# Kernel tuning notes

Hardware: AMD Instinct MI355X
Metric: run time of the kernel (lower is better)

Reference implementation:

```python
import jax, jax.numpy as jnp
import numpy as np

N = 100000   # nodes
E = 1000000  # edges (avg degree 10)
F_IN, H1, H2, C = 128, 64, 64, 16


def setup_inputs() -> dict:
    key = jax.random.key(0)
    ks = jax.random.split(key, 10)
    x = jax.random.normal(ks[0], (N, F_IN), dtype=jnp.float32)
    edge_src = jax.random.randint(ks[1], (E,), 0, N, dtype=jnp.int32)
    edge_dst = jax.random.randint(ks[2], (E,), 0, N, dtype=jnp.int32)
    # normalized-adjacency-like positive edge weights (~1/deg scale)
    edge_val = jax.random.uniform(ks[3], (E,), dtype=jnp.float32) * 0.1
    def glorot(k, fan_in, fan_out):
        s = np.float32(1.0 / np.sqrt(fan_in))
        return jax.random.normal(k, (fan_in, fan_out), dtype=jnp.float32) * s
    W1 = glorot(ks[4], F_IN, H1)
    W2 = glorot(ks[5], H1, H2)
    W3 = glorot(ks[6], H2, C)
    b1 = jnp.zeros((H1,), jnp.float32)
    b2 = jnp.zeros((H2,), jnp.float32)
    b3 = jnp.zeros((C,), jnp.float32)
    return {"x": x, "edge_val": edge_val, "W1": W1, "b1": b1,
            "W2": W2, "b2": b2, "W3": W3, "b3": b3,
            "edge_src": edge_src, "edge_dst": edge_dst}


def gcn_layer(h, W, b, edge_src, edge_dst, edge_val):
    # support = h @ W ; out = spmm(adj, support) + b
    support = h @ W                                  # [N, d_out]
    msg = support[edge_src] * edge_val[:, None]      # [E, d_out] gather + scale
    agg = jax.ops.segment_sum(msg, edge_dst, num_segments=N)  # scatter-add
    return agg + b


def reference(x, edge_val, W1, b1, W2, b2, W3, b3, edge_src, edge_dst):
    # eval mode: F.dropout(training=False) is identity
    h = jax.nn.relu(gcn_layer(x, W1, b1, edge_src, edge_dst, edge_val))
    h = jax.nn.relu(gcn_layer(h, W2, b2, edge_src, edge_dst, edge_val))
    return gcn_layer(h, W3, b3, edge_src, edge_dst, edge_val)  # [N, C] logits
```

## Files before the change

### kernel.cpp

```cpp
#include <hip/hip_runtime.h>
#include <stdint.h>

#define N_NODES 100000
#define N_EDGES 1000000
#define NBUCK 98
#define CAP 12288

typedef __attribute__((ext_vector_type(8))) __bf16 bf16x8;
typedef __attribute__((ext_vector_type(4))) float f32x4;

static __device__ __forceinline__ float bf2f(unsigned short u) {
    return __uint_as_float(((unsigned int)u) << 16);
}
static __device__ __forceinline__ unsigned short f2bf(float f) {
    unsigned int u = __float_as_uint(f);
    unsigned int r = (u + 0x7FFFu + ((u >> 16) & 1u)) >> 16;
    return (unsigned short)r;
}
static __device__ __forceinline__ float4 ld4_half(const unsigned short* p) {
    ushort4 u = *(const ushort4*)p;
    return make_float4(bf2f(u.x), bf2f(u.y), bf2f(u.z), bf2f(u.w));
}
static __device__ __forceinline__ void st4_half(unsigned short* p, float4 f) {
    ushort4 u;
    u.x = f2bf(f.x); u.y = f2bf(f.y); u.z = f2bf(f.z); u.w = f2bf(f.w);
    *(ushort4*)p = u;
}
static __device__ __forceinline__ void st8_half(unsigned short* p, const float* f) {
    int4 u;
    u.x = (int)(((unsigned)f2bf(f[0])) | (((unsigned)f2bf(f[1])) << 16));
    u.y = (int)(((unsigned)f2bf(f[2])) | (((unsigned)f2bf(f[3])) << 16));
    u.z = (int)(((unsigned)f2bf(f[4])) | (((unsigned)f2bf(f[5])) << 16));
    u.w = (int)(((unsigned)f2bf(f[6])) | (((unsigned)f2bf(f[7])) << 16));
    *(int4*)p = u;
}

static __device__ __forceinline__ float ldf(const void* p, size_t i, int bf) {
    return bf ? bf2f(((const unsigned short*)p)[i]) : ((const float*)p)[i];
}
static __device__ __forceinline__ float4 ldf4(const void* p, size_t i, int bf) {
    if (bf) return ld4_half((const unsigned short*)p + i);
    return *(const float4*)((const float*)p + i);
}

__global__ __launch_bounds__(256) void detect_kernel(const unsigned short* __restrict__ xs,
                                                     int* __restrict__ flag,
                                                     int* __restrict__ bcursor) {
    __shared__ int sz;
    if (threadIdx.x == 0) sz = 0;
    __syncthreads();
    int z = 0;
    for (int i = threadIdx.x; i < 1024; i += 256) {
        float av = fabsf(bf2f(xs[2 * i]));
        if (!(av <= 1048576.0f) || (av != 0.0f && av < 9.5367431640625e-07f)) z++;
    }
    atomicAdd(&sz, z);
    if (threadIdx.x < NBUCK) bcursor[threadIdx.x] = threadIdx.x * CAP;
    __syncthreads();
    if (threadIdx.x == 0) *flag = (sz > 256) ? 0 : 1;
}

__global__ __launch_bounds__(256) void part_kernel(const int* __restrict__ src,
                                                   const int* __restrict__ dst,
                                                   const void* __restrict__ val,
                                                   int* __restrict__ bcursor,
                                                   int2* __restrict__ part,
                                                   const int* __restrict__ flagp) {
    __shared__ int cnt[NBUCK];
    __shared__ int base[NBUCK];
    const int bf = *flagp;
    const int tid = threadIdx.x;
    const int e0 = blockIdx.x * 2048;
    for (int i = tid; i < NBUCK; i += 256) cnt[i] = 0;
    __syncthreads();
    int rank[8], bkt[8], pk[8], vb[8];
#pragma unroll
    for (int i = 0; i < 8; ++i) {
        int e = e0 + i * 256 + tid;
        bkt[i] = -1;
        if (e < N_EDGES) {
            int d = dst[e];
            int b = d >> 10;
            bkt[i] = b;
            pk[i] = src[e] | ((d & 1023) << 17);
            vb[i] = __float_as_int(ldf(val, e, bf));
            rank[i] = atomicAdd(&cnt[b], 1);
        }
    }
    __syncthreads();
    for (int i = tid; i < NBUCK; i += 256) {
        int c = cnt[i];
        base[i] = c ? atomicAdd(&bcursor[i], c) : 0;
    }
    __syncthreads();
#pragma unroll
    for (int i = 0; i < 8; ++i) {
        if (bkt[i] >= 0) part[(size_t)base[bkt[i]] + rank[i]] = make_int2(pk[i], vb[i]);
    }
}

__global__ __launch_bounds__(512) void place_kernel(const int* __restrict__ bcursor,
                                                    const int2* __restrict__ part,
                                                    int* __restrict__ row_start,
                                                    int2* __restrict__ csr_rec) {
    __shared__ int cnt[1024];
    __shared__ int sums[512];
    __shared__ int sh_s, sh_cnt, sh_total;
    const int tid = threadIdx.x;
    const int b = blockIdx.x;
    const int row0 = b << 10;
    const int nrows = min(1024, N_NODES - row0);

    if (tid < 128) sums[tid] = (tid < NBUCK) ? (bcursor[tid] - tid * CAP) : 0;
    __syncthreads();
    for (int off = 1; off < 128; off <<= 1) {
        int t = 0;
        if (tid < 128 && tid >= off) t = sums[tid - off];
        __syncthreads();
        if (tid < 128 && tid >= off) sums[tid] += t;
        __syncthreads();
    }
    if (tid == 0) {
        sh_s = (b > 0) ? sums[b - 1] : 0;
        sh_cnt = bcursor[b] - b * CAP;
        sh_total = sums[NBUCK - 1];
    }
    __syncthreads();
    const int s = sh_s;
    const int cb = sh_cnt;
    const int ps = b * CAP;
    const int total = sh_total;

    for (int i = tid; i < 1024; i += 512) cnt[i] = 0;
    __syncthreads();
    for (int j = tid; j < cb; j += 512) {
        unsigned p = (unsigned)part[ps + j].x;
        atomicAdd(&cnt[p >> 17], 1);
    }
    __syncthreads();
    int a0 = cnt[2 * tid], a1 = cnt[2 * tid + 1];
    int ts = a0 + a1;
    sums[tid] = ts;
    __syncthreads();
    for (int off = 1; off < 512; off <<= 1) {
        int t = 0;
        if (tid >= off) t = sums[tid - off];
        __syncthreads();
        if (tid >= off) sums[tid] += t;
        __syncthreads();
    }
    int excl = sums[tid] - ts;
    cnt[2 * tid] = s + excl;
    cnt[2 * tid + 1] = s + excl + a0;
    if (2 * tid < nrows)     row_start[row0 + 2 * tid] = s + excl;
    if (2 * tid + 1 < nrows) row_start[row0 + 2 * tid + 1] = s + excl + a0;
    if (b == NBUCK - 1 && tid == 0) row_start[N_NODES] = total;
    __syncthreads();
    for (int j = tid; j < cb; j += 512) {
        int2 r = part[ps + j];
        unsigned p = (unsigned)r.x;
        int pos = atomicAdd(&cnt[p >> 17], 1);
        csr_rec[pos] = make_int2((int)(p & 0x1FFFFu), r.y);
    }
}

static __device__ __forceinline__ void duo_gather64(const unsigned short* __restrict__ supc,
                                                    const int2* __restrict__ csr_rec,
                                                    int s, int b1, int e,
                                                    float a0[8], float a1[8]) {
    if (s >= e) return;
    int2 r[8];
#pragma unroll
    for (int t = 0; t < 8; ++t) r[t] = csr_rec[min(s + t, e - 1)];
    for (int j = s; j < e; j += 8) {
        int4 sp[8];
#pragma unroll
        for (int t = 0; t < 8; ++t) sp[t] = *(const int4*)(supc + (size_t)r[t].x * 64);
        float wv[8];
#pragma unroll
        for (int t = 0; t < 8; ++t) wv[t] = (j + t < e) ? __int_as_float(r[t].y) : 0.0f;
        int jn = j + 8;
        if (jn < e) {
#pragma unroll
            for (int t = 0; t < 8; ++t) r[t] = csr_rec[min(jn + t, e - 1)];
        }
#pragma unroll
        for (int t = 0; t < 8; ++t) {
            float w0 = (j + t < b1) ? wv[t] : 0.0f;
            float w1 = wv[t] - w0;
            int q[4] = {sp[t].x, sp[t].y, sp[t].z, sp[t].w};
#pragma unroll
            for (int c = 0; c < 4; ++c) {
                float flo = __uint_as_float(((unsigned)q[c]) << 16);
                float fhi = __uint_as_float(((unsigned)q[c]) & 0xffff0000u);
                a0[2 * c]     += w0 * flo; a0[2 * c + 1] += w0 * fhi;
                a1[2 * c]     += w1 * flo; a1[2 * c + 1] += w1 * fhi;
            }
        }
    }
}

static __device__ __forceinline__ void quad_gather16(const unsigned short* __restrict__ supc,
                                                     const int2* __restrict__ csr_rec,
                                                     int s, int b1, int b2, int b3, int e,
                                                     float a[4][8]) {
    if (s >= e) return;
    int2 r[8];
#pragma unroll
    for (int t = 0; t < 8; ++t) r[t] = csr_rec[min(s + t, e - 1)];
    for (int j = s; j < e; j += 8) {
        int4 sp[8];
#pragma unroll
        for (int t = 0; t < 8; ++t) sp[t] = *(const int4*)(supc + (size_t)r[t].x * 16);
        float wv[8];
#pragma unroll
        for (int t = 0; t < 8; ++t) wv[t] = (j + t < e) ? __int_as_float(r[t].y) : 0.0f;
        int jn = j + 8;
        if (jn < e) {
#pragma unroll
            for (int t = 0; t < 8; ++t) r[t] = csr_rec[min(jn + t, e - 1)];
        }
#pragma unroll
        for (int t = 0; t < 8; ++t) {
            int idx = j + t;
            float c0 = (idx < b1) ? wv[t] : 0.0f;
            float c1 = (idx < b2) ? wv[t] : 0.0f;
            float c2 = (idx < b3) ? wv[t] : 0.0f;
            float w0 = c0, w1 = c1 - c0, w2 = c2 - c1, w3 = wv[t] - c2;
            int q[4] = {sp[t].x, sp[t].y, sp[t].z, sp[t].w};
#pragma unroll
            for (int c = 0; c < 4; ++c) {
                float flo = __uint_as_float(((unsigned)q[c]) << 16);
                float fhi = __uint_as_float(((unsigned)q[c]) & 0xffff0000u);
                a[0][2 * c] += w0 * flo; a[0][2 * c + 1] += w0 * fhi;
                a[1][2 * c] += w1 * flo; a[1][2 * c + 1] += w1 * fhi;
                a[2][2 * c] += w2 * flo; a[2][2 * c + 1] += w2 * fhi;
                a[3][2 * c] += w3 * flo; a[3][2 * c + 1] += w3 * fhi;
            }
        }
    }
}

template <int K, int M, bool DYNIN>
__global__ __launch_bounds__(256) void mgemm_kernel(const void* __restrict__ hv_,
                                                    const void* __restrict__ W,
                                                    unsigned short* __restrict__ out,
                                                    const int* __restrict__ flagp) {
    constexpr int KP = K + 8;
    constexpr int NC = M / 16;
    constexpr int NK = K / 32;

    __shared__ unsigned short wt[M][KP];

    const int bf = *flagp;
    const int tid = threadIdx.x;

    for (int i = tid; i < K * M; i += 256) {
        int k = i / M, m = i % M;
        wt[m][k] = f2bf(ldf(W, i, bf));
    }
    __syncthreads();

    const int lane = tid & 63;
    const int qd = lane >> 4;
    const int ln = lane & 15;
    const int wrow = (tid >> 6) * 16;
    const int tile = blockIdx.x;

    const int row = tile * 64 + wrow + ln;
    const bool ok = row < N_NODES;

    f32x4 acc[NC];
#pragma unroll
    for (int c = 0; c < NC; ++c) acc[c] = (f32x4){0.f, 0.f, 0.f, 0.f};

#pragma unroll
    for (int ks = 0; ks < NK; ++ks) {
        bf16x8 a;
        if (ok) {
            const size_t base = (size_t)row * K + ks * 32 + qd * 8;
            if (DYNIN && !bf) {
                const float* xp = (const float*)hv_ + base;
                float4 f0 = *(const float4*)xp;
                float4 f1 = *(const float4*)(xp + 4);
                ushort4 uu[2];
                uu[0].x = f2bf(f0.x); uu[0].y = f2bf(f0.y); uu[0].z = f2bf(f0.z); uu[0].w = f2bf(f0.w);
                uu[1].x = f2bf(f1.x); uu[1].y = f2bf(f1.y); uu[1].z = f2bf(f1.z); uu[1].w = f2bf(f1.w);
                a = *(const bf16x8*)uu;
            } else {
                a = *(const bf16x8*)((const unsigned short*)hv_ + base);
            }
        } else {
            a = (bf16x8)(__bf16)0.0f;
        }
#pragma unroll
        for (int c = 0; c < NC; ++c) {
            bf16x8 b = *(const bf16x8*)&wt[c * 16 + ln][ks * 32 + qd * 8];
            acc[c] = __builtin_amdgcn_mfma_f32_16x16x32_bf16(a, b, acc[c], 0, 0, 0);
        }
    }

#pragma unroll
    for (int c = 0; c < NC; ++c) {
#pragma unroll
        for (int r = 0; r < 4; ++r) {
            int orow = tile * 64 + wrow + qd * 4 + r;
            if (orow < N_NODES) out[(size_t)orow * M + c * 16 + ln] = f2bf(acc[c][r]);
        }
    }
}

template <int MOUT>
__global__ __launch_bounds__(256) void fused_kernel(const unsigned short* __restrict__ support,
                                                    const int* __restrict__ row_start,
                                                    const int2* __restrict__ csr_rec,
                                                    const void* __restrict__ bias,
                                                    const void* __restrict__ W,
                                                    unsigned short* __restrict__ out,
                                                    const int* __restrict__ flagp) {
    constexpr int K = 64, KP = 72;
    constexpr int NC = MOUT / 16;
    constexpr int NK = 2;

    __shared__ unsigned short agg[64][KP];
    __shared__ unsigned short wt[MOUT][KP];

    const int bf = *flagp;
    const int tid = threadIdx.x;

    for (int i = tid; i < K * MOUT; i += 256) {
        int k = i / MOUT, m = i % MOUT;
        wt[m][k] = f2bf(ldf(W, i, bf));
    }
    __syncthreads();

    const int lane = tid & 63;
    const int qd = lane >> 4;
    const int ln = lane & 15;
    const int wrow = (tid >> 6) * 16;

    const int grp = tid >> 3;
    const int cc = tid & 7;
    float bias8[8];
#pragma unroll
    for (int c = 0; c < 8; ++c) bias8[c] = ldf(bias, cc * 8 + c, bf);
    const unsigned short* supc = support + cc * 8;

    const int tile = blockIdx.x;
    const int r0 = tile * 64 + grp * 2;
    int s  = row_start[min(r0 + 0, N_NODES)];
    int b1 = row_start[min(r0 + 1, N_NODES)];
    int e  = row_start[min(r0 + 2, N_NODES)];

    float a0[8], a1[8];
#pragma unroll
    for (int c = 0; c < 8; ++c) { a0[c] = bias8[c]; a1[c] = bias8[c]; }
    duo_gather64(supc, csr_rec, s, b1, e, a0, a1);
#pragma unroll
    for (int c = 0; c < 8; ++c) {
        a0[c] = fmaxf(a0[c], 0.f);
        a1[c] = fmaxf(a1[c], 0.f);
    }
    st8_half(&agg[grp * 2 + 0][cc * 8], a0);
    st8_half(&agg[grp * 2 + 1][cc * 8], a1);
    __syncthreads();

    f32x4 macc[NC];
#pragma unroll
    for (int c = 0; c < NC; ++c) macc[c] = (f32x4){0.f, 0.f, 0.f, 0.f};
#pragma unroll
    for (int ks = 0; ks < NK; ++ks) {
        bf16x8 a = *(const bf16x8*)&agg[wrow + ln][ks * 32 + qd * 8];
#pragma unroll
        for (int c = 0; c < NC; ++c) {
            bf16x8 b = *(const bf16x8*)&wt[c * 16 + ln][ks * 32 + qd * 8];
            macc[c] = __builtin_amdgcn_mfma_f32_16x16x32_bf16(a, b, macc[c], 0, 0, 0);
        }
    }

#pragma unroll
    for (int c = 0; c < NC; ++c) {
#pragma unroll
        for (int r = 0; r < 4; ++r) {
            int orow = tile * 64 + wrow + qd * 4 + r;
            if (orow < N_NODES) out[(size_t)orow * MOUT + c * 16 + ln] = f2bf(macc[c][r]);
        }
    }
}

template <bool DYNOUT>
__global__ __launch_bounds__(256) void spmm16_kernel(const unsigned short* __restrict__ support,
                                                     const int* __restrict__ row_start,
                                                     const int2* __restrict__ csr_rec,
                                                     const void* __restrict__ bias,
                                                     void* __restrict__ out_,
                                                     const int* __restrict__ flagp) {
    constexpr int M = 16;
    int bf = *flagp;
    int tid = threadIdx.x;
    int grp = tid >> 1;
    int cc = tid & 1;
    int r0 = blockIdx.x * 512 + grp * 4;
    if (r0 >= N_NODES) return;
    int s  = row_start[min(r0 + 0, N_NODES)];
    int b1 = row_start[min(r0 + 1, N_NODES)];
    int b2 = row_start[min(r0 + 2, N_NODES)];
    int b3 = row_start[min(r0 + 3, N_NODES)];
    int e  = row_start[min(r0 + 4, N_NODES)];
    float a[4][8];
#pragma unroll
    for (int k = 0; k < 4; ++k)
#pragma unroll
        for (int c = 0; c < 8; ++c) a[k][c] = ldf(bias, cc * 8 + c, bf);
    quad_gather16(support + cc * 8, csr_rec, s, b1, b2, b3, e, a);
#pragma unroll
    for (int k = 0; k < 4; ++k) {
        int row = r0 + k;
        if (row < N_NODES) {
            if (DYNOUT && !bf) {
                float* op = (float*)out_ + (size_t)row * M + cc * 8;
                *(float4*)op = make_float4(a[k][0], a[k][1], a[k][2], a[k][3]);
                *(float4*)(op + 4) = make_float4(a[k][4], a[k][5], a[k][6], a[k][7]);
            } else {
                st8_half((unsigned short*)out_ + (size_t)row * M + cc * 8, a[k]);
            }
        }
    }
}

extern "C" void kernel_launch(void* const* d_in, const int* in_sizes, int n_in,
                              void* d_out, int out_size, void* d_ws, size_t ws_size,
                              hipStream_t stream) {
    (void)in_sizes; (void)n_in; (void)out_size; (void)ws_size;
    const void* x  = d_in[0];
    const void* ev = d_in[1];
    const void* W1 = d_in[2];
    const void* b1 = d_in[3];
    const void* W2 = d_in[4];
    const void* b2 = d_in[5];
    const void* W3 = d_in[6];
    const void* b3 = d_in[7];
    const int* esrc = (const int*)d_in[8];
    const int* edst = (const int*)d_in[9];

    char* ws = (char*)d_ws;
    size_t off = 0;
    auto alloc = [&](size_t bytes) -> void* {
        void* p = ws + off;
        off = (off + bytes + 255) & ~(size_t)255;
        return p;
    };
    unsigned short* A = (unsigned short*)alloc((size_t)N_NODES * 64 * 2);
    unsigned short* B = (unsigned short*)alloc((size_t)N_NODES * 64 * 2);
    int* row_start  = (int*)alloc((size_t)(N_NODES + 1) * 4);
    int* bcursor    = (int*)alloc(512);
    int2* csr_rec   = (int2*)alloc((size_t)N_EDGES * 8);
    int* flagp      = (int*)alloc(256);
    int2* part      = (int2*)A;

    detect_kernel<<<1, 256, 0, stream>>>((const unsigned short*)x, flagp, bcursor);

    part_kernel<<<(N_EDGES + 2047) / 2048, 256, 0, stream>>>(esrc, edst, ev, bcursor, part, flagp);
    place_kernel<<<NBUCK, 512, 0, stream>>>(bcursor, part, row_start, csr_rec);

    const int NT = (N_NODES + 63) / 64;

    mgemm_kernel<128, 64, true><<<NT, 256, 0, stream>>>(x, W1, A, flagp);
    fused_kernel<64><<<NT, 256, 0, stream>>>(A, row_start, csr_rec, b1, W2, B, flagp);
    fused_kernel<16><<<NT, 256, 0, stream>>>(B, row_start, csr_rec, b2, W3, A, flagp);
    spmm16_kernel<true><<<(N_NODES + 511) / 512, 256, 0, stream>>>(A, row_start, csr_rec, b3, d_out, flagp);
}
```

Measured before the change: 244.8 us.

## Fold dtype detection into partition, stage bucket writes in LDS, persist mgemm

Drops the separate single-block detect kernel: every partition block now recomputes the bf16/fp32 detection itself, and bucket cursors are zeroed with a memset. The partition kernel first sorts its records by bucket in shared memory, so the global scatter writes become contiguous runs instead of random 8-byte stores. The first GEMM switches to a fixed grid of 512 blocks that loop over tiles, which amortises the W staging across tiles. Float-to-bf16 packing now uses a hardware paired-conversion builtin when it is available. In exchange, each partition block pays for the redundant detection and the extra LDS scan and staging.

```diff
diff --git a/kernel.cpp b/kernel.cpp
--- a/kernel.cpp
+++ b/kernel.cpp
@@ -7,6 +7,7 @@
 #define CAP 12288
 
 typedef __attribute__((ext_vector_type(8))) __bf16 bf16x8;
+typedef __attribute__((ext_vector_type(2))) __bf16 bf16x2;
 typedef __attribute__((ext_vector_type(4))) float f32x4;
 
 static __device__ __forceinline__ float bf2f(unsigned short u) {
@@ -17,63 +18,77 @@
     unsigned int r = (u + 0x7FFFu + ((u >> 16) & 1u)) >> 16;
     return (unsigned short)r;
 }
+#if defined(__has_builtin)
+#if __has_builtin(__builtin_amdgcn_cvt_pk_bf16_f32)
+#define HAS_PK_BF16 1
+#endif
+#endif
+static __device__ __forceinline__ unsigned f2bf_pk(float a, float b) {
+#ifdef HAS_PK_BF16
+    bf16x2 v = __builtin_amdgcn_cvt_pk_bf16_f32(a, b);
+    unsigned u;
+    __builtin_memcpy(&u, &v, 4);
+    return u;
+#else
+    return ((unsigned)f2bf(a)) | (((unsigned)f2bf(b)) << 16);
+#endif
+}
 static __device__ __forceinline__ float4 ld4_half(const unsigned short* p) {
     ushort4 u = *(const ushort4*)p;
     return make_float4(bf2f(u.x), bf2f(u.y), bf2f(u.z), bf2f(u.w));
 }
 static __device__ __forceinline__ void st4_half(unsigned short* p, float4 f) {
-    ushort4 u;
-    u.x = f2bf(f.x); u.y = f2bf(f.y); u.z = f2bf(f.z); u.w = f2bf(f.w);
-    *(ushort4*)p = u;
+    uint2 u;
+    u.x = f2bf_pk(f.x, f.y);
+    u.y = f2bf_pk(f.z, f.w);
+    *(uint2*)p = u;
 }
 static __device__ __forceinline__ void st8_half(unsigned short* p, const float* f) {
-    int4 u;
-    u.x = (int)(((unsigned)f2bf(f[0])) | (((unsigned)f2bf(f[1])) << 16));
-    u.y = (int)(((unsigned)f2bf(f[2])) | (((unsigned)f2bf(f[3])) << 16));
-    u.z = (int)(((unsigned)f2bf(f[4])) | (((unsigned)f2bf(f[5])) << 16));
-    u.w = (int)(((unsigned)f2bf(f[6])) | (((unsigned)f2bf(f[7])) << 16));
-    *(int4*)p = u;
+    uint4 u;
+    u.x = f2bf_pk(f[0], f[1]);
+    u.y = f2bf_pk(f[2], f[3]);
+    u.z = f2bf_pk(f[4], f[5]);
+    u.w = f2bf_pk(f[6], f[7]);
+    *(uint4*)p = u;
 }
 
 static __device__ __forceinline__ float ldf(const void* p, size_t i, int bf) {
     return bf ? bf2f(((const unsigned short*)p)[i]) : ((const float*)p)[i];
-}
-static __device__ __forceinline__ float4 ldf4(const void* p, size_t i, int bf) {
-    if (bf) return ld4_half((const unsigned short*)p + i);
-    return *(const float4*)((const float*)p + i);
-}
-
-__global__ __launch_bounds__(256) void detect_kernel(const unsigned short* __restrict__ xs,
-                                                     int* __restrict__ flag,
-                                                     int* __restrict__ bcursor) {
-    __shared__ int sz;
-    if (threadIdx.x == 0) sz = 0;
-    __syncthreads();
-    int z = 0;
-    for (int i = threadIdx.x; i < 1024; i += 256) {
-        float av = fabsf(bf2f(xs[2 * i]));
-        if (!(av <= 1048576.0f) || (av != 0.0f && av < 9.5367431640625e-07f)) z++;
-    }
-    atomicAdd(&sz, z);
-    if (threadIdx.x < NBUCK) bcursor[threadIdx.x] = threadIdx.x * CAP;
-    __syncthreads();
-    if (threadIdx.x == 0) *flag = (sz > 256) ? 0 : 1;
 }
 
 __global__ __launch_bounds__(256) void part_kernel(const int* __restrict__ src,
                                                    const int* __restrict__ dst,
                                                    const void* __restrict__ val,
+                                                   const unsigned short* __restrict__ xs,
                                                    int* __restrict__ bcursor,
                                                    int2* __restrict__ part,
-                                                   const int* __restrict__ flagp) {
+                                                   int* __restrict__ flagp) {
     __shared__ int cnt[NBUCK];
-    __shared__ int base[NBUCK];
-    const int bf = *flagp;
+    __shared__ int lbase[NBUCK];
+    __shared__ int gbase[NBUCK];
+    __shared__ int sums[128];
+    __shared__ unsigned char bb[2048];
+    __shared__ int2 buf[2048];
+    __shared__ int sz;
+
     const int tid = threadIdx.x;
     const int e0 = blockIdx.x * 2048;
+
+    if (tid == 0) sz = 0;
     for (int i = tid; i < NBUCK; i += 256) cnt[i] = 0;
     __syncthreads();
-    int rank[8], bkt[8], pk[8], vb[8];
+    int z = 0;
+    for (int i = tid; i < 1024; i += 256) {
+        float av = fabsf(bf2f(xs[2 * i]));
+        if (!(av <= 1048576.0f) || (av != 0.0f && av < 9.5367431640625e-07f)) z++;
+    }
+    if (z) atomicAdd(&sz, z);
+    __syncthreads();
+    const int bf = (sz > 256) ? 0 : 1;
+    if (blockIdx.x == 0 && tid == 0) *flagp = bf;
+
+    int rank[8], bkt[8];
+    int2 rec[8];
 #pragma unroll
     for (int i = 0; i < 8; ++i) {
         int e = e0 + i * 256 + tid;
@@ -82,20 +97,40 @@
             int d = dst[e];
             int b = d >> 10;
             bkt[i] = b;
-            pk[i] = src[e] | ((d & 1023) << 17);
-            vb[i] = __float_as_int(ldf(val, e, bf));
+            rec[i] = make_int2(src[e] | ((d & 1023) << 17),
+                               __float_as_int(ldf(val, e, bf)));
             rank[i] = atomicAdd(&cnt[b], 1);
         }
     }
     __syncthreads();
-    for (int i = tid; i < NBUCK; i += 256) {
-        int c = cnt[i];
-        base[i] = c ? atomicAdd(&bcursor[i], c) : 0;
-    }
-    __syncthreads();
+    if (tid < 128) sums[tid] = (tid < NBUCK) ? cnt[tid] : 0;
+    __syncthreads();
+    for (int off = 1; off < 128; off <<= 1) {
+        int t = 0;
+        if (tid < 128 && tid >= off) t = sums[tid - off];
+        __syncthreads();
+        if (tid < 128 && tid >= off) sums[tid] += t;
+        __syncthreads();
+    }
+    if (tid < NBUCK) {
+        lbase[tid] = sums[tid] - cnt[tid];
+        gbase[tid] = cnt[tid] ? atomicAdd(&bcursor[tid], cnt[tid]) : 0;
+    }
+    __syncthreads();
+    const int total = sums[127];
 #pragma unroll
     for (int i = 0; i < 8; ++i) {
-        if (bkt[i] >= 0) part[(size_t)base[bkt[i]] + rank[i]] = make_int2(pk[i], vb[i]);
+        if (bkt[i] >= 0) {
+            int p = lbase[bkt[i]] + rank[i];
+            buf[p] = rec[i];
+            bb[p] = (unsigned char)bkt[i];
+        }
+    }
+    __syncthreads();
+    for (int j = tid; j < total; j += 256) {
+        int b = bb[j];
+        int k = j - lbase[b];
+        part[(size_t)b * CAP + gbase[b] + k] = buf[j];
     }
 }
 
@@ -111,7 +146,7 @@
     const int row0 = b << 10;
     const int nrows = min(1024, N_NODES - row0);
 
-    if (tid < 128) sums[tid] = (tid < NBUCK) ? (bcursor[tid] - tid * CAP) : 0;
+    if (tid < 128) sums[tid] = (tid < NBUCK) ? bcursor[tid] : 0;
     __syncthreads();
     for (int off = 1; off < 128; off <<= 1) {
         int t = 0;
@@ -122,7 +157,7 @@
     }
     if (tid == 0) {
         sh_s = (b > 0) ? sums[b - 1] : 0;
-        sh_cnt = bcursor[b] - b * CAP;
+        sh_cnt = bcursor[b];
         sh_total = sums[NBUCK - 1];
     }
     __syncthreads();
@@ -249,15 +284,19 @@
     constexpr int KP = K + 8;
     constexpr int NC = M / 16;
     constexpr int NK = K / 32;
+    constexpr int NT = (N_NODES + 63) / 64;
 
     __shared__ unsigned short wt[M][KP];
 
     const int bf = *flagp;
     const int tid = threadIdx.x;
 
-    for (int i = tid; i < K * M; i += 256) {
-        int k = i / M, m = i % M;
-        wt[m][k] = f2bf(ldf(W, i, bf));
+    for (int i = tid; i < M * (K / 2); i += 256) {
+        int m = i / (K / 2);
+        int kk = i % (K / 2);
+        float va = ldf(W, (size_t)(2 * kk) * M + m, bf);
+        float vb = ldf(W, (size_t)(2 * kk + 1) * M + m, bf);
+        *(unsigned*)&wt[m][2 * kk] = f2bf_pk(va, vb);
     }
     __syncthreads();
 
@@ -265,47 +304,50 @@
     const int qd = lane >> 4;
     const int ln = lane & 15;
     const int wrow = (tid >> 6) * 16;
-    const int tile = blockIdx.x;
-
-    const int row = tile * 64 + wrow + ln;
-    const bool ok = row < N_NODES;
-
-    f32x4 acc[NC];
-#pragma unroll
-    for (int c = 0; c < NC; ++c) acc[c] = (f32x4){0.f, 0.f, 0.f, 0.f};
-
-#pragma unroll
-    for (int ks = 0; ks < NK; ++ks) {
-        bf16x8 a;
-        if (ok) {
-            const size_t base = (size_t)row * K + ks * 32 + qd * 8;
-            if (DYNIN && !bf) {
-                const float* xp = (const float*)hv_ + base;
-                float4 f0 = *(const float4*)xp;
-                float4 f1 = *(const float4*)(xp + 4);
-                ushort4 uu[2];
-                uu[0].x = f2bf(f0.x); uu[0].y = f2bf(f0.y); uu[0].z = f2bf(f0.z); uu[0].w = f2bf(f0.w);
-                uu[1].x = f2bf(f1.x); uu[1].y = f2bf(f1.y); uu[1].z = f2bf(f1.z); uu[1].w = f2bf(f1.w);
-                a = *(const bf16x8*)uu;
+
+    for (int tile = blockIdx.x; tile < NT; tile += gridDim.x) {
+        const int row = tile * 64 + wrow + ln;
+        const bool ok = row < N_NODES;
+
+        f32x4 acc[NC];
+#pragma unroll
+        for (int c = 0; c < NC; ++c) acc[c] = (f32x4){0.f, 0.f, 0.f, 0.f};
+
+#pragma unroll
+        for (int ks = 0; ks < NK; ++ks) {
+            bf16x8 a;
+            if (ok) {
+                const size_t base = (size_t)row * K + ks * 32 + qd * 8;
+                if (DYNIN && !bf) {
+                    const float* xp = (const float*)hv_ + base;
+                    float4 f0 = *(const float4*)xp;
+                    float4 f1 = *(const float4*)(xp + 4);
+                    unsigned uu[4];
+                    uu[0] = f2bf_pk(f0.x, f0.y);
+                    uu[1] = f2bf_pk(f0.z, f0.w);
+                    uu[2] = f2bf_pk(f1.x, f1.y);
+                    uu[3] = f2bf_pk(f1.z, f1.w);
+                    __builtin_memcpy(&a, uu, 16);
+                } else {
+                    a = *(const bf16x8*)((const unsigned short*)hv_ + base);
+                }
             } else {
-                a = *(const bf16x8*)((const unsigned short*)hv_ + base);
+                a = (bf16x8)(__bf16)0.0f;
             }
-        } else {
-            a = (bf16x8)(__bf16)0.0f;
-        }
+#pragma unroll
+            for (int c = 0; c < NC; ++c) {
+                bf16x8 b = *(const bf16x8*)&wt[c * 16 + ln][ks * 32 + qd * 8];
+                acc[c] = __builtin_amdgcn_mfma_f32_16x16x32_bf16(a, b, acc[c], 0, 0, 0);
+            }
+        }
+
 #pragma unroll
         for (int c = 0; c < NC; ++c) {
-            bf16x8 b = *(const bf16x8*)&wt[c * 16 + ln][ks * 32 + qd * 8];
-            acc[c] = __builtin_amdgcn_mfma_f32_16x16x32_bf16(a, b, acc[c], 0, 0, 0);
-        }
-    }
-
-#pragma unroll
-    for (int c = 0; c < NC; ++c) {
-#pragma unroll
-        for (int r = 0; r < 4; ++r) {
-            int orow = tile * 64 + wrow + qd * 4 + r;
-            if (orow < N_NODES) out[(size_t)orow * M + c * 16 + ln] = f2bf(acc[c][r]);
+#pragma unroll
+            for (int r = 0; r < 4; ++r) {
+                int orow = tile * 64 + wrow + qd * 4 + r;
+                if (orow < N_NODES) out[(size_t)orow * M + c * 16 + ln] = f2bf(acc[c][r]);
+            }
         }
     }
 }
@@ -328,9 +370,12 @@
     const int bf = *flagp;
     const int tid = threadIdx.x;
 
-    for (int i = tid; i < K * MOUT; i += 256) {
-        int k = i / MOUT, m = i % MOUT;
-        wt[m][k] = f2bf(ldf(W, i, bf));
+    for (int i = tid; i < MOUT * (K / 2); i += 256) {
+        int m = i / (K / 2);
+        int kk = i % (K / 2);
+        float va = ldf(W, (size_t)(2 * kk) * MOUT + m, bf);
+        float vb = ldf(W, (size_t)(2 * kk + 1) * MOUT + m, bf);
+        *(unsigned*)&wt[m][2 * kk] = f2bf_pk(va, vb);
     }
     __syncthreads();
 
@@ -458,14 +503,14 @@
     int* flagp      = (int*)alloc(256);
     int2* part      = (int2*)A;
 
-    detect_kernel<<<1, 256, 0, stream>>>((const unsigned short*)x, flagp, bcursor);
-
-    part_kernel<<<(N_EDGES + 2047) / 2048, 256, 0, stream>>>(esrc, edst, ev, bcursor, part, flagp);
+    hipMemsetAsync(bcursor, 0, 512, stream);
+    part_kernel<<<(N_EDGES + 2047) / 2048, 256, 0, stream>>>(
+        esrc, edst, ev, (const unsigned short*)x, bcursor, part, flagp);
     place_kernel<<<NBUCK, 512, 0, stream>>>(bcursor, part, row_start, csr_rec);
 
     const int NT = (N_NODES + 63) / 64;
 
-    mgemm_kernel<128, 64, true><<<NT, 256, 0, stream>>>(x, W1, A, flagp);
+    mgemm_kernel<128, 64, true><<<512, 256, 0, stream>>>(x, W1, A, flagp);
     fused_kernel<64><<<NT, 256, 0, stream>>>(A, row_start, csr_rec, b1, W2, B, flagp);
     fused_kernel<16><<<NT, 256, 0, stream>>>(B, row_start, csr_rec, b2, W3, A, flagp);
     spmm16_kernel<true><<<(N_NODES + 511) / 512, 256, 0, stream>>>(A, row_start, csr_rec, b3, d_out, flagp);
```

Result: no change. 247.7 us (+1.2%).
